# Kernel optimization log

Hardware: AMD Instinct MI355X
Metric: run time of the kernel (lower is better)

## Reference

```python
import jax, jax.numpy as jnp
import numpy as np

B, C, H, W = 16, 512, 32, 32
KC = C // 8  # key_channels = 64


def setup_inputs() -> dict:
    key = jax.random.key(0)
    ks = jax.random.split(key, 6)
    s_in = 1.0 / np.sqrt(C)
    return {
        "x": jax.random.normal(ks[0], (B, C, H, W), dtype=jnp.float32),
        "Wq": jax.random.normal(ks[1], (KC, C), dtype=jnp.float32) * s_in,
        "bq": jnp.zeros((KC,), dtype=jnp.float32),
        "Wk": jax.random.normal(ks[2], (KC, C), dtype=jnp.float32) * s_in,
        "bk": jnp.zeros((KC,), dtype=jnp.float32),
        "Wv": jax.random.normal(ks[3], (C, C), dtype=jnp.float32) * s_in,
        "bv": jnp.zeros((C,), dtype=jnp.float32),
        "Wo": jax.random.normal(ks[4], (C, C), dtype=jnp.float32) * s_in,
        "bo": jnp.zeros((C,), dtype=jnp.float32),
        "gamma": jnp.zeros((1,), dtype=jnp.float32),
    }


def reference(x, Wq, bq, Wk, bk, Wv, bv, Wo, bo, gamma):
    b, c, h, w = x.shape
    n = h * w
    kc = Wq.shape[0]
    xf = x.reshape(b, c, n)  # [B, C, N]
    # 1x1 convs == channel matmuls
    q = jnp.einsum('kc,bcn->bnk', Wq, xf) + bq  # [B, N, KC]
    k = jnp.einsum('kc,bcn->bkn', Wk, xf) + bk[None, :, None]  # [B, KC, N]
    v = jnp.einsum('vc,bcn->bnv', Wv, xf) + bv  # [B, N, C]
    scale = jnp.asarray(kc, x.dtype) ** -0.5
    att = jax.nn.softmax(jnp.einsum('bnk,bkm->bnm', q, k) * scale, axis=-1)  # [B, N, N]
    out = jnp.einsum('bnm,bmv->bnv', att, v)  # [B, N, C]
    out = jnp.einsum('cv,bnv->bcn', Wo, out) + bo[None, :, None]  # [B, C, N]
    out = gamma[0] * out + xf
    return out.reshape(b, c, h, w)
```

## Files before the change

kernel.cpp:

```cpp
#include <hip/hip_runtime.h>
#include <cstddef>


typedef unsigned short ushort_t;
typedef __attribute__((ext_vector_type(8))) short bf16x8;
typedef __attribute__((ext_vector_type(4))) float f32x4;
typedef __attribute__((ext_vector_type(2))) float f32x2;
typedef __attribute__((ext_vector_type(2))) unsigned u32x2;

#define QSCALE 0.18033688011112042f

__device__ __forceinline__ ushort_t f2bf_t(float f) {
  return (ushort_t)(__float_as_uint(f) >> 16);
}
__device__ __forceinline__ unsigned pk2bf(float lo, float hi) {
  return __builtin_amdgcn_perm(__float_as_uint(hi), __float_as_uint(lo),
                               0x07060302u);
}

__device__ __forceinline__ void gload16(const ushort_t* g, ushort_t* l) {
  __builtin_amdgcn_global_load_lds(
      (const __attribute__((address_space(1))) void*)g,
      (__attribute__((address_space(3))) void*)l, 16, 0, 0);
}

__device__ __forceinline__ void gemm512(
    const ushort_t* __restrict__ A, int lda,
    const ushort_t* __restrict__ B, int ldb,
    int m0, int n0, ushort_t* As, ushort_t* Bs, f32x4 (*acc)[2])
{
  const int t = threadIdx.x;
  const int lane = t & 63, quad = lane >> 4, l15 = lane & 15;
  const int w = t >> 6, wm = w >> 2, wn4 = w & 3;
  const int rr = (lane >> 3) & 7;
  const int gg = (lane & 7) ^ rr;

  #pragma unroll
  for (int i = 0; i < 4; ++i)
    #pragma unroll
    for (int j = 0; j < 2; ++j) acc[i][j] = (f32x4){0.f, 0.f, 0.f, 0.f};

  for (int k0 = 0; k0 < 512; k0 += 64) {
    __syncthreads();
    #pragma unroll
    for (int i = 0; i < 2; ++i) {
      const int mrow = w * 16 + i * 8;
      gload16(A + (size_t)(m0 + mrow + rr) * lda + k0 + gg * 8, As + mrow * 64);
      gload16(B + (size_t)(n0 + mrow + rr) * ldb + k0 + gg * 8, Bs + mrow * 64);
    }
    __syncthreads();
    #pragma unroll
    for (int kk = 0; kk < 2; ++kk) {
      const int gq = kk * 4 + quad;
      const int sg = (gq ^ (l15 & 7)) * 8;
      bf16x8 af[4], bfr[2];
      #pragma unroll
      for (int i = 0; i < 4; ++i)
        af[i] = *(const bf16x8*)(As + (wm * 64 + i * 16 + l15) * 64 + sg);
      #pragma unroll
      for (int j = 0; j < 2; ++j)
        bfr[j] = *(const bf16x8*)(Bs + (wn4 * 32 + j * 16 + l15) * 64 + sg);
      #pragma unroll
      for (int i = 0; i < 4; ++i)
        #pragma unroll
        for (int j = 0; j < 2; ++j)
          acc[i][j] = __builtin_amdgcn_mfma_f32_16x16x32_bf16(
              af[i], bfr[j], acc[i][j], 0, 0, 0);
    }
  }
  __syncthreads();
}

template <class F>
__device__ __forceinline__ void store_bf16_512(
    ushort_t* lds, ushort_t* __restrict__ out, int ldo, int m0, int n0,
    f32x4 (*acc)[2], F f)
{
  const int t = threadIdx.x;
  const int lane = t & 63, quad = lane >> 4, l15 = lane & 15;
  const int w = t >> 6, wm = w >> 2, wn4 = w & 3;
  #pragma unroll
  for (int i = 0; i < 4; ++i)
    #pragma unroll
    for (int j = 0; j < 2; ++j)
      #pragma unroll
      for (int r = 0; r < 4; ++r) {
        const int rl = wm * 64 + i * 16 + quad * 4 + r;
        const int cl = wn4 * 32 + j * 16 + l15;
        lds[rl * 136 + cl] = f2bf_t(f(i, j, r, acc[i][j][r]));
      }
  __syncthreads();
  #pragma unroll
  for (int i = 0; i < 4; ++i) {
    const int s = i * 512 + t, m = s >> 4, g = s & 15;
    const uint4 v = *(const uint4*)(lds + m * 136 + g * 8);
    *(uint4*)(out + (size_t)(m0 + m) * ldo + n0 + g * 8) = v;
  }
}

__global__ __launch_bounds__(256) void prep_x(
    const float* __restrict__ x,
    const float* __restrict__ Wq, const float* __restrict__ Wk,
    const float* __restrict__ Wv, const float* __restrict__ Wo,
    ushort_t* __restrict__ xbfT, ushort_t* __restrict__ Wqk,
    ushort_t* __restrict__ Wvb, ushort_t* __restrict__ Wob)
{
  __shared__ float T[64 * 66];
  const int t = threadIdx.x;
  if (blockIdx.y == 8) {
    const int id = blockIdx.z * 16 + blockIdx.x;
    #pragma unroll
    for (int p = 0; p < 5; ++p) {
      const int s = p * 256 + t;
      if (s < 1152) {
        const int u = id * 1152 + s;
        const int e = u * 2;
        float f0, f1;
        if (e < 32768)       { f0 = Wq[e];         f1 = Wq[e + 1]; }
        else if (e < 65536)  { f0 = Wk[e - 32768]; f1 = Wk[e - 32767]; }
        else if (e < 327680) { f0 = Wv[e - 65536]; f1 = Wv[e - 65535]; }
        else                 { f0 = Wo[e - 327680]; f1 = Wo[e - 327679]; }
        const unsigned pk = pk2bf(f0, f1);
        if (e < 65536)       *((unsigned*)Wqk + u) = pk;
        else if (e < 327680) *((unsigned*)Wvb + (u - 32768)) = pk;
        else                 *((unsigned*)Wob + (u - 163840)) = pk;
      }
    }
    return;
  }
  const int b = blockIdx.z, c0 = blockIdx.y * 64, n0 = blockIdx.x * 64;
  const float* xb = x + ((size_t)b * 512 + c0) * 1024 + n0;
  const int njf = t & 15, ci0 = t >> 4;
  #pragma unroll
  for (int p = 0; p < 4; ++p) {
    const int ci = p * 16 + ci0;
    const f32x4 v = *(const f32x4*)(xb + (size_t)ci * 1024 + njf * 4);
    float* d = &T[ci * 66 + njf * 4];
    *(f32x2*)(d)     = (f32x2){v[0], v[1]};
    *(f32x2*)(d + 2) = (f32x2){v[2], v[3]};
  }
  __syncthreads();
  const int c4 = (t & 15) * 4, nr0 = t >> 4;
  #pragma unroll
  for (int p = 0; p < 4; ++p) {
    const int nr = p * 16 + nr0;
    const float a0 = T[(c4 + 0) * 66 + nr];
    const float a1 = T[(c4 + 1) * 66 + nr];
    const float a2 = T[(c4 + 2) * 66 + nr];
    const float a3 = T[(c4 + 3) * 66 + nr];
    const u32x2 pkv = {pk2bf(a0, a1), pk2bf(a2, a3)};
    *(u32x2*)&xbfT[((size_t)b * 1024 + n0 + nr) * 512 + c0 + c4] = pkv;
  }
}

__global__ __launch_bounds__(512) void k1_fused(
    const ushort_t* __restrict__ xbfT, const ushort_t* __restrict__ Wqk,
    const ushort_t* __restrict__ Wvb,
    const float* __restrict__ bq, const float* __restrict__ bk,
    const float* __restrict__ bv,
    ushort_t* __restrict__ qkt, ushort_t* __restrict__ vt2)
{
  __shared__ __align__(16) ushort_t lds[17408];
  const unsigned lin = blockIdx.x;
  const unsigned wid = (lin & 7) * 80 + (lin >> 3);
  const int b = wid / 40, r = wid % 40;
  const int t = threadIdx.x, lane = t & 63, quad = lane >> 4, l15 = lane & 15;
  const int w = t >> 6, wm = w >> 2, wn4 = w & 3;
  f32x4 acc[4][2];
  if (r < 32) {
    const int m0 = (r >> 3) * 128, n0 = (r & 7) * 128;
    gemm512(Wvb, 512, xbfT + (size_t)b * 524288, 512, m0, n0,
            lds, lds + 8192, acc);
    float br[4][4];
    #pragma unroll
    for (int i = 0; i < 4; ++i)
      #pragma unroll
      for (int r2 = 0; r2 < 4; ++r2)
        br[i][r2] = bv[m0 + wm * 64 + i * 16 + quad * 4 + r2];
    store_bf16_512(lds, vt2 + (size_t)b * 524288, 1024, m0, n0, acc,
        [&](int i, int, int r2, float v) { return v + br[i][r2]; });
  } else {
    const int m0 = (r - 32) * 128;
    gemm512(xbfT + (size_t)b * 524288, 512, Wqk, 512, m0, 0,
            lds, lds + 8192, acc);
    float bc[2], qs[2];
    #pragma unroll
    for (int j = 0; j < 2; ++j) {
      const int col = wn4 * 32 + j * 16 + l15;
      bc[j] = (col < 64) ? bq[col] : bk[col - 64];
      qs[j] = (col < 64) ? QSCALE : 1.0f;
    }
    store_bf16_512(lds, qkt + (size_t)b * 131072, 128, m0, 0, acc,
        [&](int, int j, int, float v) { return (v + bc[j]) * qs[j]; });
  }
}

__global__ __launch_bounds__(512) void flash_attn(
    const ushort_t* __restrict__ qkt, const ushort_t* __restrict__ vt2,
    ushort_t* __restrict__ o1)
{
  __shared__ __align__(16) ushort_t buf[29696];
  __shared__ float lsum[128][2];
  ushort_t* Ks = buf;
  ushort_t* Vs = buf + 4096;
  ushort_t* Ps = buf + 20480;

  const int t = threadIdx.x;
  const int lane = t & 63, quad = lane >> 4, l15 = lane & 15;
  const int w = t >> 6, wm = w >> 1, wn2 = w & 1;
  const int rr = (lane >> 3) & 7, gg = (lane & 7) ^ rr;

  const unsigned lin = blockIdx.x;
  const unsigned wid = (lin & 7) * 32 + (lin >> 3);
  const int b  = wid >> 4;
  const int m0 = ((wid >> 1) & 7) * 128;
  const int c0 = (wid & 1) * 256;

  const ushort_t* qb = qkt + (size_t)b * 131072;
  const ushort_t* vb = vt2 + (size_t)b * 524288;

  #pragma unroll
  for (int i = 0; i < 2; ++i) {
    const int row = w * 16 + i * 8;
    gload16(qb + (size_t)(m0 + row + rr) * 128 + gg * 8, Ps + row * 64);
  }
  __syncthreads();
  bf16x8 af_q[2][2];
  #pragma unroll
  for (int kk = 0; kk < 2; ++kk) {
    const int sg = ((kk * 4 + quad) ^ (l15 & 7)) * 8;
    #pragma unroll
    for (int i = 0; i < 2; ++i)
      af_q[i][kk] = *(const bf16x8*)(Ps + (wm * 32 + i * 16 + l15) * 64 + sg);
  }

  f32x4 accO[2][8];
  #pragma unroll
  for (int i = 0; i < 2; ++i)
    #pragma unroll
    for (int j = 0; j < 8; ++j) accO[i][j] = (f32x4){0.f, 0.f, 0.f, 0.f};
  float rsum[2][4] = {{0.f, 0.f, 0.f, 0.f}, {0.f, 0.f, 0.f, 0.f}};

  ushort_t* ps_w = Ps + (wm * 32 + quad * 4) * 72 + wn2 * 32 + l15;
  const int sg0 = (quad ^ (l15 & 7)) * 8;
  const int sg1 = ((4 + quad) ^ (l15 & 7)) * 8;

  #pragma unroll 1
  for (int mc = 0; mc < 1024; mc += 64) {
    __syncthreads();
    gload16(qb + (size_t)(mc + w * 8 + rr) * 128 + 64 + gg * 8,
            Ks + (w * 8) * 64);
    #pragma unroll
    for (int i = 0; i < 4; ++i)
      gload16(vb + (size_t)(c0 + w * 32 + i * 8 + rr) * 1024 + mc + gg * 8,
              Vs + (w * 32 + i * 8) * 64);
    __syncthreads();

    f32x4 accS[2][2];
    #pragma unroll
    for (int i = 0; i < 2; ++i)
      #pragma unroll
      for (int j = 0; j < 2; ++j) accS[i][j] = (f32x4){0.f, 0.f, 0.f, 0.f};
    #pragma unroll
    for (int kk = 0; kk < 2; ++kk) {
      const int sg = kk ? sg1 : sg0;
      bf16x8 bk_[2];
      #pragma unroll
      for (int j = 0; j < 2; ++j)
        bk_[j] = *(const bf16x8*)(Ks + (wn2 * 32 + j * 16 + l15) * 64 + sg);
      #pragma unroll
      for (int i = 0; i < 2; ++i)
        #pragma unroll
        for (int j = 0; j < 2; ++j)
          accS[i][j] = __builtin_amdgcn_mfma_f32_16x16x32_bf16(
              af_q[i][kk], bk_[j], accS[i][j], 0, 0, 0);
    }
    #pragma unroll
    for (int i = 0; i < 2; ++i)
      #pragma unroll
      for (int j = 0; j < 2; ++j)
        #pragma unroll
        for (int r2 = 0; r2 < 4; ++r2) {
          const float e = __builtin_amdgcn_exp2f(accS[i][j][r2]);
          rsum[i][r2] += e;
          ps_w[(i * 16 + r2) * 72 + j * 16] = f2bf_t(e);
        }
    __syncthreads();

    #pragma unroll
    for (int kk = 0; kk < 2; ++kk) {
      const int gq = kk * 4 + quad;
      const int sgv = kk ? sg1 : sg0;
      bf16x8 ap[2], bv_[8];
      #pragma unroll
      for (int i = 0; i < 2; ++i)
        ap[i] = *(const bf16x8*)(Ps + (wm * 32 + i * 16 + l15) * 72 + gq * 8);
      #pragma unroll
      for (int j = 0; j < 8; ++j)
        bv_[j] = *(const bf16x8*)(Vs + (wn2 * 128 + j * 16 + l15) * 64 + sgv);
      #pragma unroll
      for (int i = 0; i < 2; ++i)
        #pragma unroll
        for (int j = 0; j < 8; ++j)
          accO[i][j] = __builtin_amdgcn_mfma_f32_16x16x32_bf16(
              ap[i], bv_[j], accO[i][j], 0, 0, 0);
    }
  }

  #pragma unroll
  for (int i = 0; i < 2; ++i)
    #pragma unroll
    for (int r2 = 0; r2 < 4; ++r2) {
      float s = rsum[i][r2];
      #pragma unroll
      for (int d = 1; d < 16; d <<= 1) s += __shfl_xor(s, d, 16);
      if (l15 == 0) lsum[wm * 32 + i * 16 + quad * 4 + r2][wn2] = s;
    }
  __syncthreads();

  ushort_t* fl_b = buf;
  #pragma unroll
  for (int h = 0; h < 2; ++h) {
    if ((wm >> 1) == h) {
      #pragma unroll
      for (int i = 0; i < 2; ++i)
        #pragma unroll
        for (int r2 = 0; r2 < 4; ++r2) {
          const int row = wm * 32 + i * 16 + quad * 4 + r2;
          const float inv = 1.0f / (lsum[row][0] + lsum[row][1]);
          #pragma unroll
          for (int j = 0; j < 8; ++j)
            fl_b[(row - h * 64) * 264 + wn2 * 128 + j * 16 + l15] =
                f2bf_t(accO[i][j][r2] * inv);
        }
    }
    __syncthreads();
    #pragma unroll
    for (int pp = 0; pp < 4; ++pp) {
      const int s = pp * 512 + t, m = s >> 5, g = s & 31;
      const uint4 v = *(const uint4*)(fl_b + m * 264 + g * 8);
      *(uint4*)(o1 + ((size_t)b * 1024 + m0 + h * 64 + m) * 512 + c0 + g * 8) = v;
    }
    __syncthreads();
  }
}

__global__ __launch_bounds__(512) void k4_proj(
    const ushort_t* __restrict__ Wob, const ushort_t* __restrict__ o1,
    const float* __restrict__ bo, const float* __restrict__ gamma,
    const float* __restrict__ x, float* __restrict__ out)
{
  __shared__ __align__(16) ushort_t lds[17408];
  const unsigned lin = blockIdx.x;
  const unsigned wid = (lin & 7) * 64 + (lin >> 3);
  const int b = wid >> 5, rem = wid & 31;
  const int m0 = (rem >> 3) * 128, n0 = (rem & 7) * 128;
  f32x4 acc[4][2];
  gemm512(Wob, 512, o1 + (size_t)b * 524288, 512, m0, n0,
          lds, lds + 8192, acc);
  const int t = threadIdx.x, lane = t & 63, quad = lane >> 4, l15 = lane & 15;
  const int w = t >> 6, wm = w >> 2, wn4 = w & 3;
  const float g = gamma[0];
  float br[4][4];
  #pragma unroll
  for (int i = 0; i < 4; ++i)
    #pragma unroll
    for (int r2 = 0; r2 < 4; ++r2)
      br[i][r2] = bo[m0 + wm * 64 + i * 16 + quad * 4 + r2];
  float* fl = (float*)lds;
  #pragma unroll
  for (int h = 0; h < 2; ++h) {
    if (wm == h) {
      #pragma unroll
      for (int i = 0; i < 4; ++i)
        #pragma unroll
        for (int j = 0; j < 2; ++j)
          #pragma unroll
          for (int r2 = 0; r2 < 4; ++r2)
            fl[(i * 16 + quad * 4 + r2) * 132 + wn4 * 32 + j * 16 + l15] =
                g * (acc[i][j][r2] + br[i][r2]);
    }
    __syncthreads();
    #pragma unroll
    for (int i2 = 0; i2 < 4; ++i2) {
      const int s = i2 * 512 + t, m = s >> 5, c4 = s & 31;
      f32x4 v = *(const f32x4*)(fl + m * 132 + c4 * 4);
      const size_t gi = ((size_t)b * 512 + m0 + h * 64 + m) * 1024 + n0 + c4 * 4;
      const f32x4 xr = *(const f32x4*)(x + gi);
      v += xr;
      *(f32x4*)(out + gi) = v;
    }
    __syncthreads();
  }
}

extern "C" void kernel_launch(void* const* d_in, const int* in_sizes, int n_in,
                              void* d_out, int out_size, void* d_ws, size_t ws_size,
                              hipStream_t stream) {
  const float* x     = (const float*)d_in[0];
  const float* Wq    = (const float*)d_in[1];
  const float* bq    = (const float*)d_in[2];
  const float* Wk    = (const float*)d_in[3];
  const float* bk    = (const float*)d_in[4];
  const float* Wv    = (const float*)d_in[5];
  const float* bv    = (const float*)d_in[6];
  const float* Wo    = (const float*)d_in[7];
  const float* bo    = (const float*)d_in[8];
  const float* gamma = (const float*)d_in[9];
  float* out = (float*)d_out;

  char* wsp = (char*)d_ws;
  ushort_t* xbfT   = (ushort_t*)wsp;  wsp += (size_t)16 * 1024 * 512 * 2;
  ushort_t* Wqk_bf = (ushort_t*)wsp;  wsp += (size_t)128 * 512 * 2;
  ushort_t* Wv_bf  = (ushort_t*)wsp;  wsp += (size_t)512 * 512 * 2;
  ushort_t* Wo_bf  = (ushort_t*)wsp;  wsp += (size_t)512 * 512 * 2;
  ushort_t* qkt    = (ushort_t*)wsp;  wsp += (size_t)16 * 1024 * 128 * 2;
  ushort_t* vt2    = (ushort_t*)wsp;  wsp += (size_t)16 * 512 * 1024 * 2;
  ushort_t* o1     = xbfT;

  prep_x    <<<dim3(16, 9, 16), 256, 0, stream>>>(x, Wq, Wk, Wv, Wo,
                                                  xbfT, Wqk_bf, Wv_bf, Wo_bf);
  k1_fused  <<<640, 512, 0, stream>>>(xbfT, Wqk_bf, Wv_bf, bq, bk, bv, qkt, vt2);
  flash_attn<<<256, 512, 0, stream>>>(qkt, vt2, o1);
  k4_proj   <<<512, 512, 0, stream>>>(Wo_bf, o1, bo, gamma, x, out);
}
```

Measured before the change: 168.6 us.

## Triple-buffer K/V tiles in flash attention with prefetch two iterations ahead

Replaces the synchronous load-then-sync pattern for K and V tiles with a three-slot ring buffer in LDS, issuing asynchronous global-to-LDS loads two iterations ahead and gating on vmcnt counts instead of full __syncthreads. This aims to hide global memory latency behind the QK and PV MFMA work. In exchange, LDS use per block grows from about 60KB to about 140KB, which limits occupancy. The hand-tuned waitcnt values must exactly match the number of outstanding loads per stage.

Measured after the change: 168.6 us. No clear change (+0.0%).

```diff
diff --git a/kernel.cpp b/kernel.cpp
--- a/kernel.cpp
+++ b/kernel.cpp
@@ -199,11 +199,9 @@
     const ushort_t* __restrict__ qkt, const ushort_t* __restrict__ vt2,
     ushort_t* __restrict__ o1)
 {
-  __shared__ __align__(16) ushort_t buf[29696];
+  __shared__ __align__(16) ushort_t buf[70656];
   __shared__ float lsum[128][2];
-  ushort_t* Ks = buf;
-  ushort_t* Vs = buf + 4096;
-  ushort_t* Ps = buf + 20480;
+  ushort_t* Ps = buf + 61440;
 
   const int t = threadIdx.x;
   const int lane = t & 63, quad = lane >> 4, l15 = lane & 15;
@@ -224,7 +222,9 @@
     const int row = w * 16 + i * 8;
     gload16(qb + (size_t)(m0 + row + rr) * 128 + gg * 8, Ps + row * 64);
   }
-  __syncthreads();
+  asm volatile("s_waitcnt vmcnt(0)" ::: "memory");
+  __builtin_amdgcn_sched_barrier(0);
+  __builtin_amdgcn_s_barrier();
   bf16x8 af_q[2][2];
   #pragma unroll
   for (int kk = 0; kk < 2; ++kk) {
@@ -233,6 +233,21 @@
     for (int i = 0; i < 2; ++i)
       af_q[i][kk] = *(const bf16x8*)(Ps + (wm * 32 + i * 16 + l15) * 64 + sg);
   }
+  asm volatile("s_waitcnt lgkmcnt(0)" ::: "memory");
+  __builtin_amdgcn_sched_barrier(0);
+
+  auto stage = [&](int mc, int slot) {
+    ushort_t* Kd = buf + slot * 20480;
+    ushort_t* Vd = Kd + 4096;
+    gload16(qb + (size_t)(mc + w * 8 + rr) * 128 + 64 + gg * 8,
+            Kd + (w * 8) * 64);
+    #pragma unroll
+    for (int i = 0; i < 4; ++i)
+      gload16(vb + (size_t)(c0 + w * 32 + i * 8 + rr) * 1024 + mc + gg * 8,
+              Vd + (w * 32 + i * 8) * 64);
+  };
+  stage(0, 0);
+  stage(64, 1);
 
   f32x4 accO[2][8];
   #pragma unroll
@@ -245,16 +260,23 @@
   const int sg0 = (quad ^ (l15 & 7)) * 8;
   const int sg1 = ((4 + quad) ^ (l15 & 7)) * 8;
 
+  int slot = 0;
   #pragma unroll 1
   for (int mc = 0; mc < 1024; mc += 64) {
-    __syncthreads();
-    gload16(qb + (size_t)(mc + w * 8 + rr) * 128 + 64 + gg * 8,
-            Ks + (w * 8) * 64);
-    #pragma unroll
-    for (int i = 0; i < 4; ++i)
-      gload16(vb + (size_t)(c0 + w * 32 + i * 8 + rr) * 1024 + mc + gg * 8,
-              Vs + (w * 32 + i * 8) * 64);
-    __syncthreads();
+    ushort_t* Ks = buf + slot * 20480;
+    ushort_t* Vs = Ks + 4096;
+
+    if (mc < 896) {
+      const int ns = slot < 1 ? slot + 2 : slot - 1;
+      stage(mc + 128, ns);
+      asm volatile("s_waitcnt vmcnt(10)" ::: "memory");
+    } else if (mc == 896) {
+      asm volatile("s_waitcnt vmcnt(5)" ::: "memory");
+    } else {
+      asm volatile("s_waitcnt vmcnt(0)" ::: "memory");
+    }
+    __builtin_amdgcn_sched_barrier(0);
+    __builtin_amdgcn_s_barrier();
 
     f32x4 accS[2][2];
     #pragma unroll
@@ -285,7 +307,9 @@
           rsum[i][r2] += e;
           ps_w[(i * 16 + r2) * 72 + j * 16] = f2bf_t(e);
         }
-    __syncthreads();
+    asm volatile("s_waitcnt lgkmcnt(0)" ::: "memory");
+    __builtin_amdgcn_sched_barrier(0);
+    __builtin_amdgcn_s_barrier();
 
     #pragma unroll
     for (int kk = 0; kk < 2; ++kk) {
@@ -305,6 +329,11 @@
           accO[i][j] = __builtin_amdgcn_mfma_f32_16x16x32_bf16(
               ap[i], bv_[j], accO[i][j], 0, 0, 0);
     }
+    asm volatile("s_waitcnt lgkmcnt(0)" ::: "memory");
+    __builtin_amdgcn_sched_barrier(0);
+    __builtin_amdgcn_s_barrier();
+
+    slot = slot < 2 ? slot + 1 : 0;
   }
 
   #pragma unroll
```
